# Kernel tuning notes

Measured on AMD Instinct MI355X. Metric: run time of the kernel, lower is better.

## Reference

```python
import jax, jax.numpy as jnp
import numpy as np

N_NODES = 100000
N_PER_GRAPH = 200
N_GRAPHS = N_NODES // N_PER_GRAPH
N_EDGES = 400000
F_IN = 37
H = 128          # node_hidden == transformer_hidden == fc_hidden
HEADS = 8
K_SEEDS = 75     # ceil(0.25 * 300) -> PyG GMT defaults


def _lin(key, out_d, in_d):
    kw, kb = jax.random.split(key)
    w = jax.random.normal(kw, (out_d, in_d), jnp.float32) * float(1.0 / np.sqrt(in_d))
    b = jax.random.normal(kb, (out_d,), jnp.float32) * 0.02
    return w, b


def gcn_layer(x, W, b, src, dst, n):
    # PyG GCNConv with add_self_loops and symmetric deg^-1/2 normalization
    h = x @ W.T                                   # [n, out]
    deg = jnp.ones((n,), h.dtype).at[dst].add(1.0)   # in-degree + self loop
    dinv = jax.lax.rsqrt(deg)
    msg = h[src] * (dinv[src] * dinv[dst])[:, None]  # gather + edge normalize
    agg = jnp.zeros_like(h).at[dst].add(msg)         # scatter-add
    agg = agg + h * (dinv * dinv)[:, None]           # self-loop message
    return agg + b


def attn_block(Q, K, V, fo_W, fo_b):
    # MAB core of GMT: multi-head attention (scaled by sqrt(dim_V)) + rFF residual
    B, nq, d = Q.shape
    dh = d // HEADS
    Qh = Q.reshape(B, nq, HEADS, dh)
    Kh = K.reshape(B, K.shape[1], HEADS, dh)
    Vh = V.reshape(B, V.shape[1], HEADS, dh)
    scores = jnp.einsum('bqhd,bkhd->bhqk', Qh, Kh) / jnp.sqrt(jnp.asarray(d, Q.dtype))
    A = jax.nn.softmax(scores, axis=-1)
    O = jnp.einsum('bhqk,bkhd->bqhd', A, Vh).reshape(B, nq, d)
    out = Q + O
    return out + jax.nn.relu(out @ fo_W.T + fo_b)


def setup_inputs() -> dict:
    key = jax.random.key(0)
    k = iter(jax.random.split(key, 64))
    inp = {}
    inp['herg_em'] = jax.random.normal(next(k), (1, 1280), jnp.float32)
    inp['x'] = jax.random.normal(next(k), (N_NODES, F_IN), jnp.float32)
    inp['edge_attr'] = jax.random.normal(next(k), (N_EDGES, 4), jnp.float32)
    inp['mol_rep'] = jax.random.normal(next(k), (N_GRAPHS, 11), jnp.float32)
    for i, in_d in enumerate([F_IN, H, H, H]):
        inp[f'conv_W{i}'], inp[f'conv_b{i}'] = _lin(next(k), H, in_d)
    inp['lin1_W'], inp['lin1_b'] = _lin(next(k), H, H)
    inp['lin2_W'], inp['lin2_b'] = _lin(next(k), H, H)
    inp['S1'] = jax.random.normal(next(k), (1, K_SEEDS, H), jnp.float32) * 0.1
    for p in ['pma1', 'sab', 'pma2']:
        for nm in ['fq', 'k', 'v', 'fo']:
            inp[f'{p}_{nm}_W'], inp[f'{p}_{nm}_b'] = _lin(next(k), H, H)
    inp['S2'] = jax.random.normal(next(k), (1, 1, H), jnp.float32) * 0.1
    inp['herg_lin_W'], inp['herg_lin_b'] = _lin(next(k), H, 1280)
    inp['herg_out_W'], inp['herg_out_b'] = _lin(next(k), H, 2 * H)
    inp['fc0_W'], inp['fc0_b'] = _lin(next(k), H, H)
    inp['sig_W'], inp['sig_b'] = _lin(next(k), 1, H)
    inp['edge_index'] = jax.random.randint(next(k), (2, N_EDGES), 0, N_NODES, dtype=jnp.int32)
    inp['batch'] = jnp.arange(N_NODES, dtype=jnp.int32) // N_PER_GRAPH
    return inp


def reference(herg_em, x, edge_attr, mol_rep,
              conv_W0, conv_b0, conv_W1, conv_b1, conv_W2, conv_b2, conv_W3, conv_b3,
              lin1_W, lin1_b, lin2_W, lin2_b,
              S1, pma1_fq_W, pma1_fq_b, pma1_k_W, pma1_k_b, pma1_v_W, pma1_v_b, pma1_fo_W, pma1_fo_b,
              sab_fq_W, sab_fq_b, sab_k_W, sab_k_b, sab_v_W, sab_v_b, sab_fo_W, sab_fo_b,
              S2, pma2_fq_W, pma2_fq_b, pma2_k_W, pma2_k_b, pma2_v_W, pma2_v_b, pma2_fo_W, pma2_fo_b,
              herg_lin_W, herg_lin_b, herg_out_W, herg_out_b,
              fc0_W, fc0_b, sig_W, sig_b,
              edge_index, batch):
    src, dst = edge_index[0], edge_index[1]
    n = x.shape[0]

    # stacked GCNConv + ReLU
    h = jax.nn.relu(gcn_layer(x, conv_W0, conv_b0, src, dst, n))
    for W, b in ((conv_W1, conv_b1), (conv_W2, conv_b2), (conv_W3, conv_b3)):
        h = jax.nn.relu(gcn_layer(h, W, b, src, dst, n))

    # GraphMultisetTransformer: lin1 -> GMPool_G -> SelfAtt -> GMPool_I -> lin2
    hx = h @ lin1_W.T + lin1_b                     # [N, H]
    B = N_GRAPHS

    # GMPool_G: seeds attend to GCNConv-projected keys/values (dense per graph)
    Q = jnp.broadcast_to(S1, (B, K_SEEDS, H)) @ pma1_fq_W.T + pma1_fq_b
    K = gcn_layer(hx, pma1_k_W, pma1_k_b, src, dst, n).reshape(B, N_PER_GRAPH, H)
    V = gcn_layer(hx, pma1_v_W, pma1_v_b, src, dst, n).reshape(B, N_PER_GRAPH, H)
    xb = attn_block(Q, K, V, pma1_fo_W, pma1_fo_b)     # [B, 75, H]

    # SelfAtt (SAB)
    Q = xb @ sab_fq_W.T + sab_fq_b
    K = xb @ sab_k_W.T + sab_k_b
    V = xb @ sab_v_W.T + sab_v_b
    xb = attn_block(Q, K, V, sab_fo_W, sab_fo_b)       # [B, 75, H]

    # GMPool_I: single seed, Linear keys/values
    Q = jnp.broadcast_to(S2, (B, 1, H)) @ pma2_fq_W.T + pma2_fq_b
    K = xb @ pma2_k_W.T + pma2_k_b
    V = xb @ pma2_v_W.T + pma2_v_b
    xb = attn_block(Q, K, V, pma2_fo_W, pma2_fo_b)     # [B, 1, H]

    out = xb[:, 0, :] @ lin2_W.T + lin2_b              # [B, H]

    # hERG branch
    herg = jax.nn.relu(herg_em @ herg_lin_W.T + herg_lin_b)   # [1, 128]
    herg = jnp.broadcast_to(herg, (B, herg.shape[1]))
    out = jnp.concatenate([out, herg], axis=1)                 # [B, 256]
    out = jax.nn.relu(out @ herg_out_W.T + herg_out_b)
    out = jax.nn.relu(out @ fc0_W.T + fc0_b)                   # dropout = identity (eval)
    return jax.nn.sigmoid(out @ sig_W.T + sig_b)               # [B, 1]
```

## Files before the change

### kernel.cpp

```cpp
#include <hip/hip_runtime.h>
#include <hip/hip_bf16.h>

typedef unsigned short ushort_t;
typedef unsigned int uint_t;
typedef __attribute__((ext_vector_type(8))) short short8;
typedef __attribute__((ext_vector_type(4))) float float4v;

static constexpr int NN  = 100000;
static constexpr int NE  = 400000;
static constexpr int NB  = 500;
static constexpr int NS  = 75;
static constexpr int H   = 128;
static constexpr float SCALE = 0.08838834764831845f;

union U32 { uint_t u; float f; };
__device__ __forceinline__ float bf2f(ushort_t b){ U32 t; t.u = ((uint_t)b) << 16; return t.f; }
__device__ __forceinline__ ushort_t f2bf(float f){
    U32 t; t.f = f;
    uint_t r = t.u + 0x7fffu + ((t.u >> 16) & 1u);
    return (ushort_t)(r >> 16);
}
__device__ __forceinline__ void fma8(float* a, uint4 u, float c){
    a[0] += c * bf2f((ushort_t)(u.x & 0xffff)); a[1] += c * bf2f((ushort_t)(u.x >> 16));
    a[2] += c * bf2f((ushort_t)(u.y & 0xffff)); a[3] += c * bf2f((ushort_t)(u.y >> 16));
    a[4] += c * bf2f((ushort_t)(u.z & 0xffff)); a[5] += c * bf2f((ushort_t)(u.z >> 16));
    a[6] += c * bf2f((ushort_t)(u.w & 0xffff)); a[7] += c * bf2f((ushort_t)(u.w >> 16));
}

__global__ void k_hist(int* counts, const int* __restrict__ dst, int e){
    int i = blockIdx.x*256 + threadIdx.x;
    if (i < e) atomicAdd(&counts[dst[i]], 1);
}
__global__ __launch_bounds__(256) void k_scan1(const int* __restrict__ counts,
    int* __restrict__ row_start, int* __restrict__ blockSums,
    float* __restrict__ dinv, float* __restrict__ selfc, int n){
    __shared__ int s[256];
    int t = threadIdx.x, i = blockIdx.x*256 + t;
    int v = (i < n) ? counts[i] : 0;
    s[t] = v; __syncthreads();
    #pragma unroll
    for (int off = 1; off < 256; off <<= 1){
        int add = (t >= off) ? s[t-off] : 0;
        __syncthreads();
        s[t] += add;
        __syncthreads();
    }
    if (i < n){
        row_start[i] = s[t] - v;
        float r = rsqrtf(1.f + (float)v);
        dinv[i] = r; selfc[i] = r*r;
    }
    if (t == 255) blockSums[blockIdx.x] = s[255];
}
__global__ void k_scan3(int* __restrict__ row_start, int* __restrict__ cursor,
                        const int* __restrict__ blockOff, int n, int total){
    int i = blockIdx.x*256 + threadIdx.x;
    if (i < n){
        int v = row_start[i] + blockOff[i >> 8];
        row_start[i] = v; cursor[i] = v;
    }
    if (i == 0) row_start[n] = total;
}
__global__ void k_fillcsr(const int* __restrict__ src, const int* __restrict__ dst,
    const float* __restrict__ dinv, int* cursor,
    int* __restrict__ srcs_s, float* __restrict__ ce_s, int e){
    int i = blockIdx.x*256 + threadIdx.x;
    if (i < e){
        int d = dst[i], s = src[i];
        int p = atomicAdd(&cursor[d], 1);
        srcs_s[p] = s;
        ce_s[p] = dinv[s] * dinv[d];
    }
}

struct CvtArgs { const float* w[17]; const float* w0; const float* s1; const float* s2; const float* x37; };
static constexpr int CVT_W   = 17*16384;
static constexpr int CVT_W0  = 8192;
static constexpr int CVT_S1  = 9600;
static constexpr int CVT_S2  = 128;
static constexpr int CVT_X   = NN*64;
__global__ void k_cvt_all(CvtArgs a, ushort_t* __restrict__ wbf, ushort_t* __restrict__ w0bf,
                          ushort_t* __restrict__ s1bf, ushort_t* __restrict__ s2bf,
                          ushort_t* __restrict__ xb64, int* __restrict__ counts){
    int i = blockIdx.x*256 + threadIdx.x;
    if (i < NN) counts[i] = 0;
    if (i < CVT_W){ int idx = i >> 14, off = i & 16383; wbf[i] = f2bf(a.w[idx][off]); return; }
    i -= CVT_W;
    if (i < CVT_W0){ int r = i >> 6, c = i & 63; w0bf[i] = (c < 37) ? f2bf(a.w0[r*37 + c]) : (ushort_t)0; return; }
    i -= CVT_W0;
    if (i < CVT_S1){ s1bf[i] = f2bf(a.s1[i]); return; }
    i -= CVT_S1;
    if (i < CVT_S2){ s2bf[i] = f2bf(a.s2[i]); return; }
    i -= CVT_S2;
    if (i < CVT_X){ int r = i >> 6, c = i & 63; xb64[i] = (c < 37) ? f2bf(a.x37[(size_t)r*37 + c]) : (ushort_t)0; return; }
}

__global__ __launch_bounds__(512) void k_seedq_scan2(
    const ushort_t* __restrict__ s1bf, const ushort_t* __restrict__ s2bf,
    const ushort_t* __restrict__ W1, const float* __restrict__ bias1,
    const ushort_t* __restrict__ W2q, const float* __restrict__ bias2,
    ushort_t* __restrict__ q0, ushort_t* __restrict__ q2,
    const float* __restrict__ hem, const float* __restrict__ hlW,
    const float* __restrict__ hlb, float* __restrict__ hergv,
    const int* __restrict__ blockSums, int* __restrict__ blockOff, int nb)
{
    int blk = blockIdx.x;
    int tid  = threadIdx.x;
    if (blk == 4){
        __shared__ int s[512];
        int t = tid;
        int v = (t < nb) ? blockSums[t] : 0;
        s[t] = v; __syncthreads();
        #pragma unroll
        for (int off = 1; off < 512; off <<= 1){
            int add = (t >= off) ? s[t-off] : 0;
            __syncthreads();
            s[t] += add;
            __syncthreads();
        }
        blockOff[t] = s[t] - v;
        return;
    }
    if (blk == 3){
        __shared__ float e[1280];
        for (int i = tid; i < 1280; i += 512) e[i] = hem[i];
        __syncthreads();
        if (tid < 128){
            float acc = 0.f;
            for (int k = 0; k < 1280; ++k) acc += e[k] * hlW[(size_t)tid*1280 + k];
            hergv[tid] = fmaxf(acc + hlb[tid], 0.f);
        }
        return;
    }
    if (tid >= 256) return;
    const ushort_t* x = (blk < 2) ? s1bf : s2bf;
    const ushort_t* W = (blk < 2) ? W1 : W2q;
    const float* bias = (blk < 2) ? bias1 : bias2;
    ushort_t* out = (blk < 2) ? q0 : q2;
    int M = (blk < 2) ? NS : 1;
    int base = (blk < 2) ? blk*64 : 0;
    int wid  = tid >> 6;
    int lane = tid & 63;
    int l15  = lane & 15, quad = lane >> 4;
    int row0 = base + wid*16;
    int ar   = row0 + l15; if (ar > M-1) ar = M-1;
    const short* xr = (const short*)(x + (size_t)ar*H) + quad*8;
    float4v acc[8];
    #pragma unroll
    for (int i = 0; i < 8; ++i) acc[i] = (float4v)0.f;
    #pragma unroll
    for (int kc = 0; kc < 4; ++kc){
        short8 a = *(const short8*)(xr + kc*32);
        #pragma unroll
        for (int nt = 0; nt < 8; ++nt){
            short8 b = *(const short8*)((const short*)(W + (size_t)(nt*16 + l15)*H) + kc*32 + quad*8);
            acc[nt] = __builtin_amdgcn_mfma_f32_16x16x32_bf16(a, b, acc[nt], 0, 0, 0);
        }
    }
    #pragma unroll
    for (int nt = 0; nt < 8; ++nt){
        int c = nt*16 + l15;
        float bv = bias[c];
        #pragma unroll
        for (int reg = 0; reg < 4; ++reg){
            int r = row0 + quad*4 + reg;
            if (r >= M) continue;
            out[(size_t)r*H + c] = f2bf(acc[nt][reg] + bv);
        }
    }
}

template<int NOUT, int RELU, int STAGE2, int MINW>
__global__ __launch_bounds__(256, MINW) void k_conv_fused3(
    const ushort_t* __restrict__ x,
    const int* __restrict__ row_st, const int* __restrict__ srcs,
    const float* __restrict__ ces, const float* __restrict__ selfc,
    const ushort_t* __restrict__ W, const float* __restrict__ bias0,
    const float* __restrict__ bias1,
    const ushort_t* __restrict__ W2, const float* __restrict__ bias2,
    ushort_t* __restrict__ out0, ushort_t* __restrict__ out1)
{
    __shared__ ushort_t As[32][136];
    __shared__ ushort_t Bs[(NOUT==16)?32:1][(NOUT==16)?136:1];
    const int tid = threadIdx.x;
    const int node = tid >> 3, qq = tid & 7;
    const int g = blockIdx.x*32 + node;
    float acc[16];
    #pragma unroll
    for (int i = 0; i < 16; ++i) acc[i] = 0.f;
    if (g < NN){
        const uint4* xr = (const uint4*)(x + (size_t)g*H + qq*16);
        float sc = selfc[g];
        uint4 u0 = xr[0], u1 = xr[1];
        fma8(acc+0, u0, sc); fma8(acc+8, u1, sc);
        int e = row_st[g], e1 = row_st[g+1];
        int sA = 0, sB = 0; float cA = 0.f, cB = 0.f;
        if (e < e1){ sA = srcs[e]; cA = ces[e]; }
        if (e + 1 < e1){ sB = srcs[e+1]; cB = ces[e+1]; }
        while (e + 2 <= e1){
            int sA2 = 0, sB2 = 0; float cA2 = 0.f, cB2 = 0.f;
            if (e + 2 < e1){ sA2 = srcs[e+2]; cA2 = ces[e+2]; }
            if (e + 3 < e1){ sB2 = srcs[e+3]; cB2 = ces[e+3]; }
            const uint4* pa = (const uint4*)(x + (size_t)sA*H + qq*16);
            const uint4* pb = (const uint4*)(x + (size_t)sB*H + qq*16);
            uint4 a0 = pa[0], a1 = pa[1];
            uint4 c0 = pb[0], c1 = pb[1];
            fma8(acc+0, a0, cA); fma8(acc+8, a1, cA);
            fma8(acc+0, c0, cB); fma8(acc+8, c1, cB);
            sA = sA2; sB = sB2; cA = cA2; cB = cB2;
            e += 2;
        }
        if (e < e1){
            const uint4* pa = (const uint4*)(x + (size_t)sA*H + qq*16);
            uint4 a0 = pa[0], a1 = pa[1];
            fma8(acc+0, a0, cA); fma8(acc+8, a1, cA);
        }
    }
    {
        uint_t* dst = (uint_t*)&As[node][qq*16];
        #pragma unroll
        for (int i = 0; i < 8; ++i)
            dst[i] = (uint_t)f2bf(acc[2*i]) | ((uint_t)f2bf(acc[2*i+1]) << 16);
    }
    __syncthreads();
    const int w = tid >> 6, lane = tid & 63, l15 = lane & 15, quad = lane >> 4;
    const int rt = w & 1;
    constexpr int NT = NOUT/2;
    const int ct0 = (w >> 1) * NT;
    float4v o[NT];
    #pragma unroll
    for (int t = 0; t < NT; ++t) o[t] = (float4v)0.f;
    #pragma unroll
    for (int kc = 0; kc < 4; ++kc){
        short8 a = *(const short8*)(&As[rt*16 + l15][kc*32 + quad*8]);
        #pragma unroll
        for (int t = 0; t < NT; ++t){
            short8 bfr = *(const short8*)(W + (size_t)((ct0 + t)*16 + l15)*H + kc*32 + quad*8);
            o[t] = __builtin_amdgcn_mfma_f32_16x16x32_bf16(a, bfr, o[t], 0, 0, 0);
        }
    }
    __syncthreads();
    #pragma unroll
    for (int t = 0; t < NT; ++t){
        int cg = (ct0 + t)*16 + l15;
        #pragma unroll
        for (int r = 0; r < 4; ++r){
            float v;
            if (NOUT == 8 || cg < 128){
                v = o[t][r] + bias0[cg];
                if (RELU) v = fmaxf(v, 0.f);
                As[rt*16 + quad*4 + r][cg] = f2bf(v);
            } else {
                v = o[t][r] + bias1[cg - 128];
                if (RELU) v = fmaxf(v, 0.f);
                Bs[rt*16 + quad*4 + r][cg - 128] = f2bf(v);
            }
        }
    }
    __syncthreads();
    if (STAGE2){
        float4v o2[4];
        #pragma unroll
        for (int t = 0; t < 4; ++t) o2[t] = (float4v)0.f;
        const int ct2 = (w >> 1) * 4;
        #pragma unroll
        for (int kc = 0; kc < 4; ++kc){
            short8 a = *(const short8*)(&As[rt*16 + l15][kc*32 + quad*8]);
            #pragma unroll
            for (int t = 0; t < 4; ++t){
                short8 bfr = *(const short8*)(W2 + (size_t)((ct2 + t)*16 + l15)*H + kc*32 + quad*8);
                o2[t] = __builtin_amdgcn_mfma_f32_16x16x32_bf16(a, bfr, o2[t], 0, 0, 0);
            }
        }
        __syncthreads();
        #pragma unroll
        for (int t = 0; t < 4; ++t){
            int cg = (ct2 + t)*16 + l15;
            #pragma unroll
            for (int r = 0; r < 4; ++r)
                As[rt*16 + quad*4 + r][cg] = f2bf(o2[t][r] + bias2[cg]);
        }
        __syncthreads();
    }
    if (g < NN){
        if (NOUT == 16){
            size_t kb = ((size_t)(qq >> 1)*NN + (size_t)g)*32 + (size_t)(qq & 1)*16;
            ((uint4*)(out0 + kb))[0] = *(const uint4*)&As[node][qq*16];
            ((uint4*)(out0 + kb))[1] = *(const uint4*)&As[node][qq*16 + 8];
            ((uint4*)(out1 + kb))[0] = *(const uint4*)&Bs[node][qq*16];
            ((uint4*)(out1 + kb))[1] = *(const uint4*)&Bs[node][qq*16 + 8];
        } else {
            uint4* op = (uint4*)(out0 + (size_t)g*H + qq*16);
            const uint4* sp = (const uint4*)&As[node][qq*16];
            op[0] = sp[0]; op[1] = sp[1];
        }
    }
}

__global__ __launch_bounds__(256, 8) void k_conv0b(
    const ushort_t* __restrict__ x,
    const int* __restrict__ row_st, const int* __restrict__ srcs,
    const float* __restrict__ ces, const float* __restrict__ selfc,
    const ushort_t* __restrict__ W,
    const float* __restrict__ bias,
    ushort_t* __restrict__ out)
{
    __shared__ ushort_t As[32][136];
    const int tid = threadIdx.x;
    const int node = tid >> 3, qq = tid & 7;
    const int g = blockIdx.x*32 + node;
    float acc[8];
    #pragma unroll
    for (int i = 0; i < 8; ++i) acc[i] = 0.f;
    if (g < NN){
        const uint4* xr = (const uint4*)(x + (size_t)g*64 + qq*8);
        float sc = selfc[g];
        fma8(acc, xr[0], sc);
        int e = row_st[g], e1 = row_st[g+1];
        int sA = 0, sB = 0; float cA = 0.f, cB = 0.f;
        if (e < e1){ sA = srcs[e]; cA = ces[e]; }
        if (e + 1 < e1){ sB = srcs[e+1]; cB = ces[e+1]; }
        while (e + 2 <= e1){
            int sA2 = 0, sB2 = 0; float cA2 = 0.f, cB2 = 0.f;
            if (e + 2 < e1){ sA2 = srcs[e+2]; cA2 = ces[e+2]; }
            if (e + 3 < e1){ sB2 = srcs[e+3]; cB2 = ces[e+3]; }
            uint4 a0 = *(const uint4*)(x + (size_t)sA*64 + qq*8);
            uint4 c0 = *(const uint4*)(x + (size_t)sB*64 + qq*8);
            fma8(acc, a0, cA);
            fma8(acc, c0, cB);
            sA = sA2; sB = sB2; cA = cA2; cB = cB2;
            e += 2;
        }
        if (e < e1){
            uint4 a0 = *(const uint4*)(x + (size_t)sA*64 + qq*8);
            fma8(acc, a0, cA);
        }
    }
    {
        uint_t* dst = (uint_t*)&As[node][qq*8];
        #pragma unroll
        for (int i = 0; i < 4; ++i)
            dst[i] = (uint_t)f2bf(acc[2*i]) | ((uint_t)f2bf(acc[2*i+1]) << 16);
    }
    __syncthreads();
    const int w = tid >> 6, lane = tid & 63, l15 = lane & 15, quad = lane >> 4;
    const int rt = w & 1;
    const int ct0 = (w >> 1) * 4;
    float4v o[4];
    #pragma unroll
    for (int t = 0; t < 4; ++t) o[t] = (float4v)0.f;
    #pragma unroll
    for (int kc = 0; kc < 2; ++kc){
        short8 a = *(const short8*)(&As[rt*16 + l15][kc*32 + quad*8]);
        #pragma unroll
        for (int t = 0; t < 4; ++t){
            short8 bfr = *(const short8*)(W + (size_t)((ct0 + t)*16 + l15)*64 + kc*32 + quad*8);
            o[t] = __builtin_amdgcn_mfma_f32_16x16x32_bf16(a, bfr, o[t], 0, 0, 0);
        }
    }
    __syncthreads();
    #pragma unroll
    for (int t = 0; t < 4; ++t){
        int cg = (ct0 + t)*16 + l15;
        #pragma unroll
        for (int r = 0; r < 4; ++r)
            As[rt*16 + quad*4 + r][cg] = f2bf(fmaxf(o[t][r] + bias[cg], 0.f));
    }
    __syncthreads();
    if (g < NN){
        uint4* op = (uint4*)(out + (size_t)g*H + qq*16);
        const uint4* sp = (const uint4*)&As[node][qq*16];
        op[0] = sp[0]; op[1] = sp[1];
    }
}

template<int NK, int HM>
__global__ __launch_bounds__(256) void k_attn_mfma(
    const ushort_t* __restrict__ Q, int qbs,
    const ushort_t* __restrict__ K, const ushort_t* __restrict__ V,
    ushort_t* __restrict__ out, int nq)
{
    constexpr int NKT = (NK + 15) / 16;
    constexpr int NKC = (NK + 31) / 32;
    __shared__ ushort_t Ks[2][208][24];
    __shared__ ushort_t Vs[2][16][232];
    __shared__ ushort_t Ps[4][16][232];
    int b = blockIdx.x >> 2, hp = blockIdx.x & 3;
    int h0 = hp*2;
    int tid = threadIdx.x;
    {
        uint_t* p = (uint_t*)&Ps[0][0][0];
        for (int i = tid; i < 4*16*232/2; i += 256) p[i] = 0;
    }
    const ushort_t* Kb = HM ? (K + ((size_t)hp*NB + b)*NK*32)
                            : (K + (size_t)b*NK*H + h0*16);
    for (int idx = tid; idx < NK*8; idx += 256){
        int key = idx >> 3, p = idx & 7;
        int hh = p >> 2, dl = (p & 3)*4;
        const uint_t* src = HM ? (const uint_t*)(Kb + (size_t)key*32 + hh*16 + dl)
                               : (const uint_t*)(Kb + (size_t)key*H + hh*16 + dl);
        uint_t* d = (uint_t*)&Ks[hh][key][dl];
        d[0] = src[0]; d[1] = src[1];
    }
    const ushort_t* Vb = HM ? (V + ((size_t)hp*NB + b)*NK*32)
                            : (V + (size_t)b*NK*H + h0*16);
    for (int idx = tid; idx < NK*8; idx += 256){
        int key = idx >> 3, p = idx & 7;
        int hh = p >> 2, dl = (p & 3)*4;
        const ushort_t* src = HM ? (Vb + (size_t)key*32 + hh*16 + dl)
                                 : (Vb + (size_t)key*H + hh*16 + dl);
        Vs[hh][dl+0][key] = src[0];
        Vs[hh][dl+1][key] = src[1];
        Vs[hh][dl+2][key] = src[2];
        Vs[hh][dl+3][key] = src[3];
    }
    for (int idx = tid; idx < 2*16*(232-NK); idx += 256){
        int key = NK + idx % (232-NK), r = idx / (232-NK);
        Vs[r>>4][r&15][key] = 0;
    }
    __syncthreads();

    int w = tid >> 6, lane = tid & 63;
    int hh = w >> 1, half = w & 1;
    int h = h0 + hh;
    int l15 = lane & 15, quad = lane >> 4;
    bool klow = (quad < 2);
    int nqt = (nq + 15) >> 4;
    int split = (nqt + 1) >> 1;
    int qt0 = half ? split : 0;
    int qt1 = half ? nqt : split;
    for (int qt = qt0; qt < qt1; ++qt){
        int qr = qt*16 + l15; if (qr > nq-1) qr = nq-1;
        short8 av = *(const short8*)(Q + (size_t)b*qbs + (size_t)qr*H + h*16 + (quad & 1)*8);
        short8 zero8 = (short8)0;
        short8 afrag = klow ? av : zero8;
        float4v s[NKT];
        #pragma unroll
        for (int kt = 0; kt < NKT; ++kt){
            short8 bv = *(const short8*)(&Ks[hh][kt*16 + l15][(quad & 1)*8]);
            short8 bfrag = klow ? bv : zero8;
            s[kt] = __builtin_amdgcn_mfma_f32_16x16x32_bf16(afrag, bfrag, (float4v)0.f, 0, 0, 0);
        }
        float mx[4] = {-1e30f, -1e30f, -1e30f, -1e30f};
        #pragma unroll
        for (int kt = 0; kt < NKT; ++kt){
            if (kt*16 + l15 >= NK){ s[kt][0]=-1e30f; s[kt][1]=-1e30f; s[kt][2]=-1e30f; s[kt][3]=-1e30f; }
            #pragma unroll
            for (int r = 0; r < 4; ++r) mx[r] = fmaxf(mx[r], s[kt][r]);
        }
        #pragma unroll
        for (int off = 1; off < 16; off <<= 1){
            #pragma unroll
            for (int r = 0; r < 4; ++r) mx[r] = fmaxf(mx[r], __shfl_xor(mx[r], off));
        }
        float sum[4] = {0.f, 0.f, 0.f, 0.f};
        #pragma unroll
        for (int kt = 0; kt < NKT; ++kt){
            #pragma unroll
            for (int r = 0; r < 4; ++r){
                float e = __expf((s[kt][r] - mx[r]) * SCALE);
                sum[r] += e;
                Ps[w][quad*4 + r][kt*16 + l15] = f2bf(e);
            }
        }
        #pragma unroll
        for (int off = 1; off < 16; off <<= 1){
            #pragma unroll
            for (int r = 0; r < 4; ++r) sum[r] += __shfl_xor(sum[r], off);
        }
        float4v o = (float4v)0.f;
        #pragma unroll
        for (int kc = 0; kc < NKC; ++kc){
            short8 pa = *(const short8*)(&Ps[w][l15][kc*32 + quad*8]);
            short8 vb = *(const short8*)(&Vs[hh][l15][kc*32 + quad*8]);
            o = __builtin_amdgcn_mfma_f32_16x16x32_bf16(pa, vb, o, 0, 0, 0);
        }
        #pragma unroll
        for (int r = 0; r < 4; ++r){
            int row = qt*16 + quad*4 + r;
            if (row < nq){
                float qv = bf2f(Q[(size_t)b*qbs + (size_t)row*H + h*16 + l15]);
                out[((size_t)b*nq + row)*H + h*16 + l15] = f2bf(qv + o[r] / sum[r]);
            }
        }
    }
}

struct TailArgs {
    const ushort_t* xA; const ushort_t* q2;
    const ushort_t* p1foW; const float* p1fob;
    const ushort_t* sfqW;  const float* sfqb;
    const ushort_t* skW;   const float* skb;
    const ushort_t* svW;   const float* svb;
    const ushort_t* sfoW;  const float* sfob;
    const ushort_t* p2kW;  const float* p2kb;
    const ushort_t* p2vW;  const float* p2vb;
    const ushort_t* p2foW; const float* p2fob;
    const ushort_t* lin2W; const float* lin2b;
    const float* hergv;
    const float* hoW; const float* hob;
    const float* fcW; const float* fcb;
    const float* sW;  const float* sb;
    float* outp;
};

__global__ __launch_bounds__(512, 4) void k_graph_tail(TailArgs a){
    __shared__ ushort_t bufA[83*136];
    __shared__ ushort_t bufB[80*136];
    __shared__ ushort_t bufC[80*136];
    __shared__ ushort_t vt4[64*104];
    const int b = blockIdx.x, tid = threadIdx.x;
    const int w = tid >> 6, lane = tid & 63, l15 = lane & 15, quad = lane >> 4;
    ushort_t* psw = (w == 0) ? bufA + 10200 :
                    (w == 1) ? bufA + 10712 :
                    (w == 2) ? bufB + 10200 : bufC + 10200;

    for (int i = tid; i < 64*104/2; i += 512) ((uint_t*)vt4)[i] = 0u;
    {
        const ushort_t* xg = a.xA + (size_t)b*NS*H;
        for (int i = tid; i < NS*16; i += 512){
            int row = i >> 4, q = i & 15;
            *(uint4*)(bufA + row*136 + q*8) = *(const uint4*)(xg + (size_t)row*H + q*8);
        }
    }
    __syncthreads();

    for (int rt = w; rt < 5; rt += 8){
        float4v o[8];
        #pragma unroll
        for (int i = 0; i < 8; ++i) o[i] = (float4v)0.f;
        #pragma unroll
        for (int kc = 0; kc < 4; ++kc){
            short8 av = *(const short8*)(bufA + (rt*16 + l15)*136 + kc*32 + quad*8);
            #pragma unroll
            for (int ct = 0; ct < 8; ++ct){
                short8 bv = *(const short8*)((const short*)(a.p1foW + (size_t)(ct*16 + l15)*H) + kc*32 + quad*8);
                o[ct] = __builtin_amdgcn_mfma_f32_16x16x32_bf16(av, bv, o[ct], 0, 0, 0);
            }
        }
        #pragma unroll
        for (int ct = 0; ct < 8; ++ct){
            int c = ct*16 + l15; float bb = a.p1fob[c];
            #pragma unroll
            for (int r = 0; r < 4; ++r){
                int row = rt*16 + quad*4 + r;
                float res = bf2f(bufA[row*136 + c]);
                bufA[row*136 + c] = f2bf(fmaxf(o[ct][r] + bb, 0.f) + res);
            }
        }
    }
    __syncthreads();

    for (int job = w; job < 40; job += 8){
        int rt = job >> 3, ct = job & 7;
        float4v o = (float4v)0.f;
        #pragma unroll
        for (int kc = 0; kc < 4; ++kc){
            short8 av = *(const short8*)(bufA + (rt*16 + l15)*136 + kc*32 + quad*8);
            short8 bv = *(const short8*)((const short*)(a.sfqW + (size_t)(ct*16 + l15)*H) + kc*32 + quad*8);
            o = __builtin_amdgcn_mfma_f32_16x16x32_bf16(av, bv, o, 0, 0, 0);
        }
        int c = ct*16 + l15; float bb = a.sfqb[c];
        #pragma unroll
        for (int r = 0; r < 4; ++r)
            bufB[(rt*16 + quad*4 + r)*136 + c] = f2bf(o[r] + bb);
    }
    for (int job = w; job < 40; job += 8){
        int rt = job >> 3, ct = job & 7;
        float4v o = (float4v)0.f;
        #pragma unroll
        for (int kc = 0; kc < 4; ++kc){
            short8 av = *(const short8*)(bufA + (rt*16 + l15)*136 + kc*32 + quad*8);
            short8 bv = *(const short8*)((const short*)(a.skW + (size_t)(ct*16 + l15)*H) + kc*32 + quad*8);
            o = __builtin_amdgcn_mfma_f32_16x16x32_bf16(av, bv, o, 0, 0, 0);
        }
        int c = ct*16 + l15; float bb = a.skb[c];
        #pragma unroll
        for (int r = 0; r < 4; ++r)
            bufC[(rt*16 + quad*4 + r)*136 + c] = f2bf(o[r] + bb);
    }
    __syncthreads();

    for (int pass = 0; pass < 2; ++pass){
        int hbase = pass*4;
        for (int job = w; job < 20; job += 8){
            int rt = job >> 2, ctl = job & 3;
            int ct = hbase + ctl;
            float4v o = (float4v)0.f;
            #pragma unroll
            for (int kc = 0; kc < 4; ++kc){
                short8 av = *(const short8*)(bufA + (rt*16 + l15)*136 + kc*32 + quad*8);
                short8 bv = *(const short8*)((const short*)(a.svW + (size_t)(ct*16 + l15)*H) + kc*32 + quad*8);
                o = __builtin_amdgcn_mfma_f32_16x16x32_bf16(av, bv, o, 0, 0, 0);
            }
            int c = ct*16 + l15; float bb = a.svb[c];
            #pragma unroll
            for (int r = 0; r < 4; ++r){
                int key = rt*16 + quad*4 + r;
                if (key < NS) vt4[(ctl*16 + l15)*104 + key] = f2bf(o[r] + bb);
            }
        }
        __syncthreads();
        if (w < 4){
            int hl = w, h = hbase + w;
            short8 zero8 = (short8)0;
            bool klow = (quad < 2);
            for (int qt = 0; qt < 5; ++qt){
                short8 av = *(const short8*)(bufB + (qt*16 + l15)*136 + h*16 + (quad & 1)*8);
                short8 afrag = klow ? av : zero8;
                float4v s[5];
                #pragma unroll
                for (int kt = 0; kt < 5; ++kt){
                    short8 bv = *(const short8*)(bufC + (kt*16 + l15)*136 + h*16 + (quad & 1)*8);
                    short8 bfrag = klow ? bv : zero8;
                    s[kt] = __builtin_amdgcn_mfma_f32_16x16x32_bf16(afrag, bfrag, (float4v)0.f, 0, 0, 0);
                }
                float mx[4] = {-1e30f, -1e30f, -1e30f, -1e30f};
                #pragma unroll
                for (int kt = 0; kt < 5; ++kt){
                    if (kt*16 + l15 >= NS){ s[kt][0]=-1e30f; s[kt][1]=-1e30f; s[kt][2]=-1e30f; s[kt][3]=-1e30f; }
                    #pragma unroll
                    for (int r = 0; r < 4; ++r) mx[r] = fmaxf(mx[r], s[kt][r]);
                }
                #pragma unroll
                for (int off = 1; off < 16; off <<= 1){
                    #pragma unroll
                    for (int r = 0; r < 4; ++r) mx[r] = fmaxf(mx[r], __shfl_xor(mx[r], off));
                }
                float sum[4] = {0.f, 0.f, 0.f, 0.f};
                float4v o = (float4v)0.f;
                #pragma unroll
                for (int kc = 0; kc < 3; ++kc){
                    #pragma unroll
                    for (int t2 = 0; t2 < 2; ++t2){
                        int kt = kc*2 + t2;
                        #pragma unroll
                        for (int r = 0; r < 4; ++r){
                            float e = 0.f;
                            if (kt < 5){ e = __expf((s[kt][r] - mx[r]) * SCALE); sum[r] += e; }
                            psw[(quad*4 + r)*32 + t2*16 + l15] = f2bf(e);
                        }
                    }
                    short8 pa = *(const short8*)(psw + l15*32 + quad*8);
                    short8 vb = *(const short8*)(vt4 + (hl*16 + l15)*104 + kc*32 + quad*8);
                    o = __builtin_amdgcn_mfma_f32_16x16x32_bf16(pa, vb, o, 0, 0, 0);
                }
                #pragma unroll
                for (int off = 1; off < 16; off <<= 1){
                    #pragma unroll
                    for (int r = 0; r < 4; ++r) sum[r] += __shfl_xor(sum[r], off);
                }
                #pragma unroll
                for (int r = 0; r < 4; ++r){
                    int row = qt*16 + quad*4 + r;
                    if (row < NS){
                        float qv = bf2f(bufB[row*136 + h*16 + l15]);
                        bufB[row*136 + h*16 + l15] = f2bf(qv + o[r] / sum[r]);
                    }
                }
            }
        }
        __syncthreads();
    }

    for (int job = w; job < 40; job += 8){
        int rt = job >> 3, ct = job & 7;
        float4v o = (float4v)0.f;
        #pragma unroll
        for (int kc = 0; kc < 4; ++kc){
            short8 av = *(const short8*)(bufB + (rt*16 + l15)*136 + kc*32 + quad*8);
            short8 bv = *(const short8*)((const short*)(a.sfoW + (size_t)(ct*16 + l15)*H) + kc*32 + quad*8);
            o = __builtin_amdgcn_mfma_f32_16x16x32_bf16(av, bv, o, 0, 0, 0);
        }
        int c = ct*16 + l15; float bb = a.sfob[c];
        #pragma unroll
        for (int r = 0; r < 4; ++r){
            int row = rt*16 + quad*4 + r;
            bufA[row*136 + c] = f2bf(fmaxf(o[r] + bb, 0.f) + bf2f(bufB[row*136 + c]));
        }
    }
    __syncthreads();

    for (int job = w; job < 40; job += 8){
        int rt = job >> 3, ct = job & 7;
        float4v o = (float4v)0.f;
        #pragma unroll
        for (int kc = 0; kc < 4; ++kc){
            short8 av = *(const short8*)(bufA + (rt*16 + l15)*136 + kc*32 + quad*8);
            short8 bv = *(const short8*)((const short*)(a.p2kW + (size_t)(ct*16 + l15)*H) + kc*32 + quad*8);
            o = __builtin_amdgcn_mfma_f32_16x16x32_bf16(av, bv, o, 0, 0, 0);
        }
        int c = ct*16 + l15; float bb = a.p2kb[c];
        #pragma unroll
        for (int r = 0; r < 4; ++r)
            bufC[(rt*16 + quad*4 + r)*136 + c] = f2bf(o[r] + bb);
    }
    for (int job = w; job < 40; job += 8){
        int rt = job >> 3, ct = job & 7;
        float4v o = (float4v)0.f;
        #pragma unroll
        for (int kc = 0; kc < 4; ++kc){
            short8 av = *(const short8*)(bufA + (rt*16 + l15)*136 + kc*32 + quad*8);
            short8 bv = *(const short8*)((const short*)(a.p2vW + (size_t)(ct*16 + l15)*H) + kc*32 + quad*8);
            o = __builtin_amdgcn_mfma_f32_16x16x32_bf16(av, bv, o, 0, 0, 0);
        }
        int c = ct*16 + l15; float bb = a.p2vb[c];
        #pragma unroll
        for (int r = 0; r < 4; ++r)
            bufB[(rt*16 + quad*4 + r)*136 + c] = f2bf(o[r] + bb);
    }
    __syncthreads();

    {
        int t = tid;
        char* sb8 = (char*)bufA;
        float* sc       = (float*)sb8;
        float* sumh     = (float*)(sb8 + 2432);
        ushort_t* xa    = (ushort_t*)(sb8 + 2464);
        ushort_t* xb3   = (ushort_t*)(sb8 + 2720);
        float* tt       = (float*)(sb8 + 2976);
        float* v256     = (float*)(sb8 + 3488);
        float* red      = (float*)(sb8 + 4512);
        if (t < 256){
            int h = t >> 5, l32 = t & 31;
            const ushort_t* qr = a.q2 + h*16;
            for (int k = l32; k < NS; k += 32){
                float s = 0.f;
                #pragma unroll
                for (int d = 0; d < 16; ++d) s += bf2f(qr[d]) * bf2f(bufC[k*136 + h*16 + d]);
                sc[h*76 + k] = s;
            }
        }
        __syncthreads();
        if (t < 128){
            int hh = t >> 4, i = t & 15;
            float mx = -1e30f;
            for (int k = i; k < NS; k += 16) mx = fmaxf(mx, sc[hh*76 + k]);
            #pragma unroll
            for (int off = 1; off < 16; off <<= 1) mx = fmaxf(mx, __shfl_xor(mx, off));
            float sm = 0.f;
            for (int k = i; k < NS; k += 16){
                float e = __expf((sc[hh*76 + k] - mx) * SCALE);
                sc[hh*76 + k] = e;
                sm += e;
            }
            #pragma unroll
            for (int off = 1; off < 16; off <<= 1) sm += __shfl_xor(sm, off);
            if (i == 0) sumh[hh] = sm;
        }
        __syncthreads();
        if (t < 128){
            int hh = t >> 4;
            float o = 0.f;
            for (int k = 0; k < NS; ++k) o += sc[hh*76 + k] * bf2f(bufB[k*136 + t]);
            xa[t] = f2bf(bf2f(a.q2[t]) + o / sumh[hh]);
        }
        __syncthreads();
        if (t < 128){
            float acc = 0.f;
            const ushort_t* wr = a.p2foW + (size_t)t*H;
            for (int k = 0; k < H; ++k) acc += bf2f(xa[k]) * bf2f(wr[k]);
            xb3[t] = f2bf(fmaxf(acc + a.p2fob[t], 0.f) + bf2f(xa[t]));
        }
        __syncthreads();
        if (t < 128){
            float acc = 0.f;
            const ushort_t* wr = a.lin2W + (size_t)t*H;
            for (int k = 0; k < H; ++k) acc += bf2f(xb3[k]) * bf2f(wr[k]);
            v256[t] = acc + a.lin2b[t];
            v256[128 + t] = a.hergv[t];
        }
        __syncthreads();
        if (t < 128){
            float acc = 0.f;
            const float* wr = a.hoW + (size_t)t*256;
            for (int k = 0; k < 256; ++k) acc += v256[k] * wr[k];
            tt[t] = fmaxf(acc + a.hob[t], 0.f);
        }
        __syncthreads();
        if (t < 128){
            float acc = 0.f;
            const float* wr = a.fcW + (size_t)t*128;
            for (int k = 0; k < 128; ++k) acc += tt[k] * wr[k];
            float uv = fmaxf(acc + a.fcb[t], 0.f);
            red[t] = uv * a.sW[t];
        }
        __syncthreads();
        for (int s = 64; s > 0; s >>= 1){
            if (t < s) red[t] += red[t + s];
            __syncthreads();
        }
        if (t == 0){
            float logit = red[0] + a.sb[0];
            a.outp[b] = 1.f / (1.f + expf(-logit));
        }
    }
}

extern "C" void kernel_launch(void* const* d_in, const int* in_sizes, int n_in,
                              void* d_out, int out_size, void* d_ws, size_t ws_size,
                              hipStream_t stream)
{
    (void)in_sizes; (void)n_in; (void)out_size; (void)ws_size;
    const float* herg_em = (const float*)d_in[0];
    const float* x_in    = (const float*)d_in[1];
    const float* convW[4] = {(const float*)d_in[4], (const float*)d_in[6], (const float*)d_in[8], (const float*)d_in[10]};
    const float* convB[4] = {(const float*)d_in[5], (const float*)d_in[7], (const float*)d_in[9], (const float*)d_in[11]};
    const float* lin1W = (const float*)d_in[12]; const float* lin1b = (const float*)d_in[13];
    const float* lin2W = (const float*)d_in[14]; const float* lin2b = (const float*)d_in[15];
    const float* S1    = (const float*)d_in[16];
    const float* p1fqW = (const float*)d_in[17]; const float* p1fqb = (const float*)d_in[18];
    const float* p1kW  = (const float*)d_in[19]; const float* p1kb  = (const float*)d_in[20];
    const float* p1vW  = (const float*)d_in[21]; const float* p1vb  = (const float*)d_in[22];
    const float* p1foW = (const float*)d_in[23]; const float* p1fob = (const float*)d_in[24];
    const float* sfqW  = (const float*)d_in[25]; const float* sfqb  = (const float*)d_in[26];
    const float* skW   = (const float*)d_in[27]; const float* skb   = (const float*)d_in[28];
    const float* svW   = (const float*)d_in[29]; const float* svb   = (const float*)d_in[30];
    const float* sfoW  = (const float*)d_in[31]; const float* sfob  = (const float*)d_in[32];
    const float* p2fqW = (const float*)d_in[33]; const float* p2fqb = (const float*)d_in[34];
    const float* p2kW  = (const float*)d_in[35]; const float* p2kb  = (const float*)d_in[36];
    const float* p2vW  = (const float*)d_in[37]; const float* p2vb  = (const float*)d_in[38];
    const float* p2foW = (const float*)d_in[39]; const float* p2fob = (const float*)d_in[40];
    const float* S2    = (const float*)d_in[41];
    const float* hlW   = (const float*)d_in[42]; const float* hlb   = (const float*)d_in[43];
    const float* hoW   = (const float*)d_in[44]; const float* hob   = (const float*)d_in[45];
    const float* fcW   = (const float*)d_in[46]; const float* fcb   = (const float*)d_in[47];
    const float* sW    = (const float*)d_in[48]; const float* sb    = (const float*)d_in[49];
    const int*  ei    = (const int*)d_in[50];
    const int*  esrc  = ei;
    const int*  edst  = ei + NE;
    float* outp = (float*)d_out;

    char* WS = (char*)d_ws;
    int*   counts = (int*)(WS + 0);
    int*   cursor = (int*)(WS + 400384);
    int*   row_st = (int*)(WS + 800768);
    int*   bSums  = (int*)(WS + 1201152);
    int*   bOff   = (int*)(WS + 1203200);
    float* dinv   = (float*)(WS + 1205248);
    float* selfc  = (float*)(WS + 1605632);
    int*   srcs_s = (int*)(WS + 2005632);
    float* ce_s   = (float*)(WS + 3605632);
    ushort_t* wbf = (ushort_t*)(WS + 5205632);
    ushort_t* w0bf= (ushort_t*)(WS + 5762688);
    ushort_t* s1bf= (ushort_t*)(WS + 5779072);
    ushort_t* s2bf= (ushort_t*)(WS + 5798272);
    ushort_t* q0  = (ushort_t*)(WS + 5798528);
    ushort_t* q2  = (ushort_t*)(WS + 5817728);
    float* hergv  = (float*)(WS + 5817984);
    ushort_t* xb64= (ushort_t*)(WS + 6074496);
    ushort_t* b0  = (ushort_t*)(WS + 18874496);
    ushort_t* b1  = (ushort_t*)(WS + 44474496);
    ushort_t* b2  = (ushort_t*)(WS + 70074496);
    ushort_t* xA  = (ushort_t*)(WS + 95674496);

    const int gN   = (NN + 255)/256;
    const int gE   = (NE + 255)/256;
    const int gC   = (NN + 31)/32;

    CvtArgs ca;
    ca.w[0]=convW[1]; ca.w[1]=convW[2]; ca.w[2]=convW[3]; ca.w[3]=lin1W; ca.w[4]=lin2W;
    ca.w[5]=p1kW; ca.w[6]=p1vW; ca.w[7]=p1foW;
    ca.w[8]=sfqW; ca.w[9]=skW; ca.w[10]=svW; ca.w[11]=sfoW;
    ca.w[12]=p2kW; ca.w[13]=p2vW; ca.w[14]=p2foW; ca.w[15]=p1fqW; ca.w[16]=p2fqW;
    ca.w0 = convW[0]; ca.s1 = S1; ca.s2 = S2; ca.x37 = x_in;
    const int cvtTotal = CVT_W + CVT_W0 + CVT_S1 + CVT_S2 + CVT_X;
    k_cvt_all<<<(cvtTotal + 255)/256, 256, 0, stream>>>(ca, wbf, w0bf, s1bf, s2bf, xb64, counts);

    k_hist  <<<gE, 256, 0, stream>>>(counts, edst, NE);
    k_scan1 <<<gN, 256, 0, stream>>>(counts, row_st, bSums, dinv, selfc, NN);
    k_seedq_scan2<<<5, 512, 0, stream>>>(s1bf, s2bf, wbf + (size_t)15*16384, p1fqb,
                                   wbf + (size_t)16*16384, p2fqb, q0, q2,
                                   herg_em, hlW, hlb, hergv,
                                   bSums, bOff, gN);
    k_scan3 <<<gN, 256, 0, stream>>>(row_st, cursor, bOff, NN, NE);
    k_fillcsr<<<gE, 256, 0, stream>>>(esrc, edst, dinv, cursor, srcs_s, ce_s, NE);

    k_conv0b<<<gC, 256, 0, stream>>>(xb64, row_st, srcs_s, ce_s, selfc, w0bf, convB[0], b0);
    k_conv_fused3<8,1,0,8><<<gC, 256, 0, stream>>>(b0, row_st, srcs_s, ce_s, selfc,
        wbf + (size_t)0*16384, convB[1], nullptr, nullptr, nullptr, b1, nullptr);
    k_conv_fused3<8,1,0,8><<<gC, 256, 0, stream>>>(b1, row_st, srcs_s, ce_s, selfc,
        wbf + (size_t)1*16384, convB[2], nullptr, nullptr, nullptr, b0, nullptr);
    k_conv_fused3<8,1,1,8><<<gC, 256, 0, stream>>>(b0, row_st, srcs_s, ce_s, selfc,
        wbf + (size_t)2*16384, convB[3], nullptr, wbf + (size_t)3*16384, lin1b, b1, nullptr);
    k_conv_fused3<16,0,0,4><<<gC, 256, 0, stream>>>(b1, row_st, srcs_s, ce_s, selfc,
        wbf + (size_t)5*16384, p1kb, p1vb, nullptr, nullptr, b2, b0);
    k_attn_mfma<200,1><<<NB*4, 256, 0, stream>>>(q0, 0, b2, b0, xA, NS);

    TailArgs ta;
    ta.xA = xA; ta.q2 = q2;
    ta.p1foW = wbf + (size_t)7*16384;  ta.p1fob = p1fob;
    ta.sfqW  = wbf + (size_t)8*16384;  ta.sfqb  = sfqb;
    ta.skW   = wbf + (size_t)9*16384;  ta.skb   = skb;
    ta.svW   = wbf + (size_t)10*16384; ta.svb   = svb;
    ta.sfoW  = wbf + (size_t)11*16384; ta.sfob  = sfob;
    ta.p2kW  = wbf + (size_t)12*16384; ta.p2kb  = p2kb;
    ta.p2vW  = wbf + (size_t)13*16384; ta.p2vb  = p2vb;
    ta.p2foW = wbf + (size_t)14*16384; ta.p2fob = p2fob;
    ta.lin2W = wbf + (size_t)4*16384;  ta.lin2b = lin2b;
    ta.hergv = hergv;
    ta.hoW = hoW; ta.hob = hob;
    ta.fcW = fcW; ta.fcb = fcb;
    ta.sW = sW; ta.sb = sb;
    ta.outp = outp;
    k_graph_tail<<<NB, 512, 0, stream>>>(ta);
}
```

Before: 655.1 us.

## Fuse PMA1 attention into graph tail kernel, dropping separate attention launch

Removes the standalone per-(graph, head-pair) attention kernel and computes PMA1 attention inside k_graph_tail, looping over four head pairs per block and writing results straight into shared memory. This avoids one launch and the global write and read of the intermediate attention output xA. In exchange, each tail block now does all eight heads serially across 10 work items per head pair on 8 waves, so load balance is uneven. Parallelism also drops from 2000 blocks to 500, and extra syncthreads are added. The P tile is built incrementally per 32-key chunk in a small per-wave buffer.

```diff
diff --git a/kernel.cpp b/kernel.cpp
--- a/kernel.cpp
+++ b/kernel.cpp
@@ -374,120 +374,9 @@
     }
 }
 
-template<int NK, int HM>
-__global__ __launch_bounds__(256) void k_attn_mfma(
-    const ushort_t* __restrict__ Q, int qbs,
-    const ushort_t* __restrict__ K, const ushort_t* __restrict__ V,
-    ushort_t* __restrict__ out, int nq)
-{
-    constexpr int NKT = (NK + 15) / 16;
-    constexpr int NKC = (NK + 31) / 32;
-    __shared__ ushort_t Ks[2][208][24];
-    __shared__ ushort_t Vs[2][16][232];
-    __shared__ ushort_t Ps[4][16][232];
-    int b = blockIdx.x >> 2, hp = blockIdx.x & 3;
-    int h0 = hp*2;
-    int tid = threadIdx.x;
-    {
-        uint_t* p = (uint_t*)&Ps[0][0][0];
-        for (int i = tid; i < 4*16*232/2; i += 256) p[i] = 0;
-    }
-    const ushort_t* Kb = HM ? (K + ((size_t)hp*NB + b)*NK*32)
-                            : (K + (size_t)b*NK*H + h0*16);
-    for (int idx = tid; idx < NK*8; idx += 256){
-        int key = idx >> 3, p = idx & 7;
-        int hh = p >> 2, dl = (p & 3)*4;
-        const uint_t* src = HM ? (const uint_t*)(Kb + (size_t)key*32 + hh*16 + dl)
-                               : (const uint_t*)(Kb + (size_t)key*H + hh*16 + dl);
-        uint_t* d = (uint_t*)&Ks[hh][key][dl];
-        d[0] = src[0]; d[1] = src[1];
-    }
-    const ushort_t* Vb = HM ? (V + ((size_t)hp*NB + b)*NK*32)
-                            : (V + (size_t)b*NK*H + h0*16);
-    for (int idx = tid; idx < NK*8; idx += 256){
-        int key = idx >> 3, p = idx & 7;
-        int hh = p >> 2, dl = (p & 3)*4;
-        const ushort_t* src = HM ? (Vb + (size_t)key*32 + hh*16 + dl)
-                                 : (Vb + (size_t)key*H + hh*16 + dl);
-        Vs[hh][dl+0][key] = src[0];
-        Vs[hh][dl+1][key] = src[1];
-        Vs[hh][dl+2][key] = src[2];
-        Vs[hh][dl+3][key] = src[3];
-    }
-    for (int idx = tid; idx < 2*16*(232-NK); idx += 256){
-        int key = NK + idx % (232-NK), r = idx / (232-NK);
-        Vs[r>>4][r&15][key] = 0;
-    }
-    __syncthreads();
-
-    int w = tid >> 6, lane = tid & 63;
-    int hh = w >> 1, half = w & 1;
-    int h = h0 + hh;
-    int l15 = lane & 15, quad = lane >> 4;
-    bool klow = (quad < 2);
-    int nqt = (nq + 15) >> 4;
-    int split = (nqt + 1) >> 1;
-    int qt0 = half ? split : 0;
-    int qt1 = half ? nqt : split;
-    for (int qt = qt0; qt < qt1; ++qt){
-        int qr = qt*16 + l15; if (qr > nq-1) qr = nq-1;
-        short8 av = *(const short8*)(Q + (size_t)b*qbs + (size_t)qr*H + h*16 + (quad & 1)*8);
-        short8 zero8 = (short8)0;
-        short8 afrag = klow ? av : zero8;
-        float4v s[NKT];
-        #pragma unroll
-        for (int kt = 0; kt < NKT; ++kt){
-            short8 bv = *(const short8*)(&Ks[hh][kt*16 + l15][(quad & 1)*8]);
-            short8 bfrag = klow ? bv : zero8;
-            s[kt] = __builtin_amdgcn_mfma_f32_16x16x32_bf16(afrag, bfrag, (float4v)0.f, 0, 0, 0);
-        }
-        float mx[4] = {-1e30f, -1e30f, -1e30f, -1e30f};
-        #pragma unroll
-        for (int kt = 0; kt < NKT; ++kt){
-            if (kt*16 + l15 >= NK){ s[kt][0]=-1e30f; s[kt][1]=-1e30f; s[kt][2]=-1e30f; s[kt][3]=-1e30f; }
-            #pragma unroll
-            for (int r = 0; r < 4; ++r) mx[r] = fmaxf(mx[r], s[kt][r]);
-        }
-        #pragma unroll
-        for (int off = 1; off < 16; off <<= 1){
-            #pragma unroll
-            for (int r = 0; r < 4; ++r) mx[r] = fmaxf(mx[r], __shfl_xor(mx[r], off));
-        }
-        float sum[4] = {0.f, 0.f, 0.f, 0.f};
-        #pragma unroll
-        for (int kt = 0; kt < NKT; ++kt){
-            #pragma unroll
-            for (int r = 0; r < 4; ++r){
-                float e = __expf((s[kt][r] - mx[r]) * SCALE);
-                sum[r] += e;
-                Ps[w][quad*4 + r][kt*16 + l15] = f2bf(e);
-            }
-        }
-        #pragma unroll
-        for (int off = 1; off < 16; off <<= 1){
-            #pragma unroll
-            for (int r = 0; r < 4; ++r) sum[r] += __shfl_xor(sum[r], off);
-        }
-        float4v o = (float4v)0.f;
-        #pragma unroll
-        for (int kc = 0; kc < NKC; ++kc){
-            short8 pa = *(const short8*)(&Ps[w][l15][kc*32 + quad*8]);
-            short8 vb = *(const short8*)(&Vs[hh][l15][kc*32 + quad*8]);
-            o = __builtin_amdgcn_mfma_f32_16x16x32_bf16(pa, vb, o, 0, 0, 0);
-        }
-        #pragma unroll
-        for (int r = 0; r < 4; ++r){
-            int row = qt*16 + quad*4 + r;
-            if (row < nq){
-                float qv = bf2f(Q[(size_t)b*qbs + (size_t)row*H + h*16 + l15]);
-                out[((size_t)b*nq + row)*H + h*16 + l15] = f2bf(qv + o[r] / sum[r]);
-            }
-        }
-    }
-}
-
 struct TailArgs {
-    const ushort_t* xA; const ushort_t* q2;
+    const ushort_t* Khm; const ushort_t* Vhm;
+    const ushort_t* q0;  const ushort_t* q2;
     const ushort_t* p1foW; const float* p1fob;
     const ushort_t* sfqW;  const float* sfqb;
     const ushort_t* skW;   const float* skb;
@@ -511,20 +400,98 @@
     __shared__ ushort_t vt4[64*104];
     const int b = blockIdx.x, tid = threadIdx.x;
     const int w = tid >> 6, lane = tid & 63, l15 = lane & 15, quad = lane >> 4;
-    ushort_t* psw = (w == 0) ? bufA + 10200 :
-                    (w == 1) ? bufA + 10712 :
-                    (w == 2) ? bufB + 10200 : bufC + 10200;
-
-    for (int i = tid; i < 64*104/2; i += 512) ((uint_t*)vt4)[i] = 0u;
-    {
-        const ushort_t* xg = a.xA + (size_t)b*NS*H;
-        for (int i = tid; i < NS*16; i += 512){
-            int row = i >> 4, q = i & 15;
-            *(uint4*)(bufA + row*136 + q*8) = *(const uint4*)(xg + (size_t)row*H + q*8);
-        }
-    }
-    __syncthreads();
-
+
+    for (int i = tid; i < 2*16*32; i += 512){
+        int hh2 = i >> 9, rr = (i >> 5) & 15, kk = 200 + (i & 31);
+        bufC[(hh2*16 + rr)*232 + kk] = 0;
+    }
+    for (int hp = 0; hp < 4; ++hp){
+        __syncthreads();
+        const ushort_t* Kb = a.Khm + ((size_t)hp*NB + b)*(size_t)200*32;
+        for (int idx = tid; idx < 200*8; idx += 512){
+            int key = idx >> 3, p = idx & 7;
+            int hh = p >> 2, dl = (p & 3)*4;
+            const uint_t* src = (const uint_t*)(Kb + (size_t)key*32 + hh*16 + dl);
+            uint_t* d = (uint_t*)&bufB[(hh*208 + key)*24 + dl];
+            d[0] = src[0]; d[1] = src[1];
+        }
+        const ushort_t* Vb = a.Vhm + ((size_t)hp*NB + b)*(size_t)200*32;
+        for (int idx = tid; idx < 200*8; idx += 512){
+            int key = idx >> 3, p = idx & 7;
+            int hh = p >> 2, dl = (p & 3)*4;
+            const ushort_t* src = Vb + (size_t)key*32 + hh*16 + dl;
+            bufC[(hh*16 + dl+0)*232 + key] = src[0];
+            bufC[(hh*16 + dl+1)*232 + key] = src[1];
+            bufC[(hh*16 + dl+2)*232 + key] = src[2];
+            bufC[(hh*16 + dl+3)*232 + key] = src[3];
+        }
+        __syncthreads();
+        for (int j = w; j < 10; j += 8){
+            int hl = j / 5, qt = j % 5;
+            int gh = hp*2 + hl;
+            ushort_t* psw = vt4 + w*512;
+            int qr = qt*16 + l15; if (qr > NS-1) qr = NS-1;
+            short8 av = *(const short8*)(a.q0 + (size_t)qr*H + gh*16 + (quad & 1)*8);
+            short8 zero8 = (short8)0;
+            bool klow = (quad < 2);
+            short8 afrag = klow ? av : zero8;
+            float4v s[13];
+            #pragma unroll
+            for (int kt = 0; kt < 13; ++kt){
+                short8 bv = *(const short8*)(&bufB[(hl*208 + kt*16 + l15)*24 + (quad & 1)*8]);
+                short8 bfrag = klow ? bv : zero8;
+                s[kt] = __builtin_amdgcn_mfma_f32_16x16x32_bf16(afrag, bfrag, (float4v)0.f, 0, 0, 0);
+            }
+            float mx[4] = {-1e30f, -1e30f, -1e30f, -1e30f};
+            #pragma unroll
+            for (int kt = 0; kt < 13; ++kt){
+                if (kt*16 + l15 >= 200){ s[kt][0]=-1e30f; s[kt][1]=-1e30f; s[kt][2]=-1e30f; s[kt][3]=-1e30f; }
+                #pragma unroll
+                for (int r = 0; r < 4; ++r) mx[r] = fmaxf(mx[r], s[kt][r]);
+            }
+            #pragma unroll
+            for (int off = 1; off < 16; off <<= 1){
+                #pragma unroll
+                for (int r = 0; r < 4; ++r) mx[r] = fmaxf(mx[r], __shfl_xor(mx[r], off));
+            }
+            float sum[4] = {0.f, 0.f, 0.f, 0.f};
+            float4v o = (float4v)0.f;
+            #pragma unroll
+            for (int kc = 0; kc < 7; ++kc){
+                #pragma unroll
+                for (int t2 = 0; t2 < 2; ++t2){
+                    int kt = kc*2 + t2;
+                    #pragma unroll
+                    for (int r = 0; r < 4; ++r){
+                        float e = 0.f;
+                        if (kt < 13){ e = __expf((s[kt][r] - mx[r]) * SCALE); sum[r] += e; }
+                        psw[(quad*4 + r)*32 + t2*16 + l15] = f2bf(e);
+                    }
+                }
+                short8 pa = *(const short8*)(psw + l15*32 + quad*8);
+                short8 vb = *(const short8*)(&bufC[(hl*16 + l15)*232 + kc*32 + quad*8]);
+                o = __builtin_amdgcn_mfma_f32_16x16x32_bf16(pa, vb, o, 0, 0, 0);
+            }
+            #pragma unroll
+            for (int off = 1; off < 16; off <<= 1){
+                #pragma unroll
+                for (int r = 0; r < 4; ++r) sum[r] += __shfl_xor(sum[r], off);
+            }
+            #pragma unroll
+            for (int r = 0; r < 4; ++r){
+                int row = qt*16 + quad*4 + r;
+                if (row < NS){
+                    float qv = bf2f(a.q0[(size_t)row*H + gh*16 + l15]);
+                    bufA[row*136 + gh*16 + l15] = f2bf(qv + o[r] / sum[r]);
+                }
+            }
+        }
+    }
+    __syncthreads();
+
+    if (w >= 5){
+        for (int i = tid - 320; i < 64*104/2; i += 192) ((uint_t*)vt4)[i] = 0u;
+    }
     for (int rt = w; rt < 5; rt += 8){
         float4v o[8];
         #pragma unroll
@@ -602,6 +569,9 @@
         }
         __syncthreads();
         if (w < 4){
+            ushort_t* psw = (w == 0) ? bufA + 10200 :
+                            (w == 1) ? bufA + 10712 :
+                            (w == 2) ? bufB + 10200 : bufC + 10200;
             int hl = w, h = hbase + w;
             short8 zero8 = (short8)0;
             bool klow = (quad < 2);
@@ -852,7 +822,6 @@
     ushort_t* b0  = (ushort_t*)(WS + 18874496);
     ushort_t* b1  = (ushort_t*)(WS + 44474496);
     ushort_t* b2  = (ushort_t*)(WS + 70074496);
-    ushort_t* xA  = (ushort_t*)(WS + 95674496);
 
     const int gN   = (NN + 255)/256;
     const int gE   = (NE + 255)/256;
@@ -885,10 +854,9 @@
         wbf + (size_t)2*16384, convB[3], nullptr, wbf + (size_t)3*16384, lin1b, b1, nullptr);
     k_conv_fused3<16,0,0,4><<<gC, 256, 0, stream>>>(b1, row_st, srcs_s, ce_s, selfc,
         wbf + (size_t)5*16384, p1kb, p1vb, nullptr, nullptr, b2, b0);
-    k_attn_mfma<200,1><<<NB*4, 256, 0, stream>>>(q0, 0, b2, b0, xA, NS);
 
     TailArgs ta;
-    ta.xA = xA; ta.q2 = q2;
+    ta.Khm = b2; ta.Vhm = b0; ta.q0 = q0; ta.q2 = q2;
     ta.p1foW = wbf + (size_t)7*16384;  ta.p1fob = p1fob;
     ta.sfqW  = wbf + (size_t)8*16384;  ta.sfqb  = sfqb;
     ta.skW   = wbf + (size_t)9*16384;  ta.skb   = skb;
```

Result: no change. 642.8 us (-1.9%).
